# Optimization experiments

Hardware: AMD Instinct MI355X
Metric: run time of the kernel (lower is better)

Reference implementation:

```python
import jax, jax.numpy as jnp
import numpy as np

PADDING = 2  # matches init_kwargs; kernel_size = 2*PADDING + 1 -> no circular wrap in roll trick


def setup_inputs() -> dict:
    key = jax.random.key(0)
    k1, k2, k3 = jax.random.split(key, 3)
    x = jax.random.normal(k1, (16, 512, 4096), dtype=jnp.float32)
    weight = jax.random.normal(k2, (512, 512, 5), dtype=jnp.float32)
    bias = jax.random.normal(k3, (512,), dtype=jnp.float32)
    return {"x": x, "weight": weight, "bias": bias}


def reference(x, weight, bias):
    # Original torch module: pad(p,p) -> cat of roll(n-p) copies -> slice -> matmul.
    # Index algebra: out[b,o,t] = sum_{c,n} w[o,c,n] * xpad[b,c, t + 2p - n],
    # which (with kernel_size == 2p+1, so no circular wraparound) is a true
    # convolution, i.e. cross-correlation with the kernel flipped along taps.
    w_flipped = jnp.flip(weight, axis=-1)  # [O, I, K]
    y = jax.lax.conv_general_dilated(
        x, w_flipped,
        window_strides=(1,),
        padding=[(PADDING, PADDING)],
        dimension_numbers=("NCH", "OIH", "NCH"),
    )  # [B, O, T]
    return y + bias[None, :, None]
```

## Files before the change

kernel.cpp:

```cpp
#include <hip/hip_runtime.h>
#include <hip/hip_bf16.h>

typedef __attribute__((ext_vector_type(8))) short short8;
typedef __attribute__((ext_vector_type(4))) float f32x4;

#define B_   16
#define O_   512
#define C_   512
#define T_   4096
#define TP   (T_ + 32)
#define KT   5
#define BM   128
#define BN   512
#define BK   32
#define NCHUNK (C_/BK)
#define AFR  40
#define BGR  33

__device__ __forceinline__ void gload_lds16(const void* g, void* l) {
    __builtin_amdgcn_global_load_lds(
        (const __attribute__((address_space(1))) unsigned int*)g,
        (__attribute__((address_space(3))) unsigned int*)l, 16, 0, 0);
}

__global__ void prep_kernel(const float* __restrict__ w,
                            unsigned short* __restrict__ wb,
                            unsigned short* __restrict__ xt) {
    int bid = blockIdx.x;
    if (bid < 5120) {
        int e   = bid * 256 + threadIdx.x;
        int n   = e / (O_ * C_);
        int rem = e % (O_ * C_);
        int o   = rem / C_;
        int c   = rem % C_;
        float v = w[((size_t)o * C_ + c) * KT + n];
        __hip_bfloat16 h = __float2bfloat16(v);
        wb[e] = *reinterpret_cast<unsigned short*>(&h);
    } else {
        int i = (bid - 5120) * 256 + threadIdx.x;
        int b = i / (32 * C_);
        int r = (i / C_) % 32;
        int c = i % C_;
        int tp = (r < 16) ? r : (T_ + r);
        xt[((size_t)b * TP + tp) * C_ + c] = 0;
    }
}

__global__ void xtrans_kernel(const float* __restrict__ x, unsigned short* __restrict__ xt) {
    __shared__ float tile[64][65];
    int b  = blockIdx.z;
    int c0 = blockIdx.y * 64;
    int t0 = blockIdx.x * 64;
    const float* xb = x + ((size_t)b * C_ + c0) * T_ + t0;
#pragma unroll
    for (int p = 0; p < 4; ++p) {
        int idx = p * 256 + threadIdx.x;
        int cl = idx >> 4;
        int tj = (idx & 15) << 2;
        float4 v = *reinterpret_cast<const float4*>(xb + (size_t)cl * T_ + tj);
        tile[cl][tj + 0] = v.x;
        tile[cl][tj + 1] = v.y;
        tile[cl][tj + 2] = v.z;
        tile[cl][tj + 3] = v.w;
    }
    __syncthreads();
    unsigned short* xtb = xt + ((size_t)b * TP + 16 + t0) * C_ + c0;
#pragma unroll
    for (int p = 0; p < 2; ++p) {
        int g  = p * 256 + threadIdx.x;
        int tl = g >> 3;
        int cj = (g & 7) << 3;
        unsigned short tmp[8];
#pragma unroll
        for (int i = 0; i < 8; ++i) {
            __hip_bfloat16 h = __float2bfloat16(tile[cj + i][tl]);
            tmp[i] = *reinterpret_cast<unsigned short*>(&h);
        }
        *reinterpret_cast<short8*>(xtb + (size_t)tl * C_ + cj) =
            *reinterpret_cast<const short8*>(tmp);
    }
}

__global__ __launch_bounds__(512, 2) void conv_gemm_kernel(
        const unsigned short* __restrict__ wb,
        const unsigned short* __restrict__ xt,
        const float* __restrict__ bias,
        float* __restrict__ out) {
    __shared__ unsigned short a_lds[2][AFR * 512];
    __shared__ unsigned short b_lds[2][BGR * 512];

    int bid = blockIdx.x;
    int swz = (bid & 7) * 64 + (bid >> 3);
    int o0  = (swz & 3) * BM;
    int t0  = ((swz >> 2) & 7) * BN;
    int b   = swz >> 5;

    int tid  = threadIdx.x;
    int lane = tid & 63;
    int wid  = tid >> 6;
    int lr   = lane & 15;
    int lg   = lane >> 4;

    int bo[KT][4];
#pragma unroll
    for (int n = 0; n < KT; ++n)
#pragma unroll
        for (int ni = 0; ni < 4; ++ni) {
            int row = wid * 64 + ni * 16 + lr + 4 - n;
            bo[n][ni] = row * 32 + ((lg ^ ((row >> 1) & 3)) << 3);
        }

    f32x4 acc[8][4];
#pragma unroll
    for (int mi = 0; mi < 8; ++mi)
#pragma unroll
        for (int ni = 0; ni < 4; ++ni)
            acc[mi][ni] = (f32x4)0.0f;

    const unsigned short* ag = wb + (size_t)(o0 + lr) * C_ + lg * 8;
    int c8 = (lane & 3) ^ ((lane >> 3) & 3);
    const unsigned short* bg = xt + ((size_t)b * TP + (t0 + 14 + (lane >> 2))) * C_ + c8 * 8;

#pragma unroll
    for (int f = wid; f < AFR; f += 8)
        gload_lds16(ag + (size_t)((f >> 3) * O_ + (f & 7) * 16) * C_, &a_lds[0][f * 512]);
#pragma unroll
    for (int j = wid; j < BGR; j += 8)
        gload_lds16(bg + (size_t)(j * 16) * C_, &b_lds[0][j * 512]);
    asm volatile("s_waitcnt vmcnt(0)" ::: "memory");
    __builtin_amdgcn_s_barrier();

    for (int chunk = 0; chunk < NCHUNK; ++chunk) {
        int cur = chunk & 1;
        int c1  = (chunk + 1) * BK;
        bool pf = (chunk + 1 < NCHUNK);

#pragma unroll
        for (int n = 0; n < KT; ++n) {
            short8 af[8], bf[4];
#pragma unroll
            for (int mi = 0; mi < 8; ++mi)
                af[mi] = *reinterpret_cast<const short8*>(
                    &a_lds[cur][(n * 8 + mi) * 512 + lane * 8]);
#pragma unroll
            for (int ni = 0; ni < 4; ++ni)
                bf[ni] = *reinterpret_cast<const short8*>(&b_lds[cur][bo[n][ni]]);

            if (pf) {
                int f = n * 8 + wid;
                gload_lds16(ag + (size_t)((f >> 3) * O_ + (f & 7) * 16) * C_ + c1,
                            &a_lds[cur ^ 1][f * 512]);
                int j = n * 8 + wid;
                if (j < BGR)
                    gload_lds16(bg + (size_t)(j * 16) * C_ + c1, &b_lds[cur ^ 1][j * 512]);
            }

            __builtin_amdgcn_s_barrier();

            __builtin_amdgcn_s_setprio(1);
#pragma unroll
            for (int mi = 0; mi < 8; ++mi)
#pragma unroll
                for (int ni = 0; ni < 4; ++ni)
                    acc[mi][ni] = __builtin_amdgcn_mfma_f32_16x16x32_bf16(
                        af[mi], bf[ni], acc[mi][ni], 0, 0, 0);
            __builtin_amdgcn_s_setprio(0);
        }

        asm volatile("s_waitcnt vmcnt(0)" ::: "memory");
        __builtin_amdgcn_s_barrier();
    }

#pragma unroll
    for (int mi = 0; mi < 8; ++mi) {
#pragma unroll
        for (int ni = 0; ni < 4; ++ni) {
            int orow = o0 + mi * 16 + lg * 4;
            int tcol = t0 + wid * 64 + ni * 16 + lr;
#pragma unroll
            for (int r = 0; r < 4; ++r) {
                out[((size_t)b * O_ + orow + r) * T_ + tcol] =
                    acc[mi][ni][r] + bias[orow + r];
            }
        }
    }
}

extern "C" void kernel_launch(void* const* d_in, const int* in_sizes, int n_in,
                              void* d_out, int out_size, void* d_ws, size_t ws_size,
                              hipStream_t stream) {
    const float* x    = (const float*)d_in[0];
    const float* w    = (const float*)d_in[1];
    const float* bias = (const float*)d_in[2];
    float* out        = (float*)d_out;

    unsigned short* wb  = (unsigned short*)d_ws;
    unsigned short* xtp = wb + (size_t)KT * O_ * C_;

    prep_kernel<<<6144, 256, 0, stream>>>(w, wb, xtp);
    xtrans_kernel<<<dim3(T_ / 64, C_ / 64, B_), 256, 0, stream>>>(x, xtp);
    conv_gemm_kernel<<<512, 512, 0, stream>>>(wb, xtp, bias, out);
}
```

Baseline: 189.0 us.

## Retile conv GEMM to 256x256 blocks with 4-stage per-tap LDS pipeline

```diff
diff --git a/kernel.cpp b/kernel.cpp
--- a/kernel.cpp
+++ b/kernel.cpp
@@ -10,12 +10,7 @@
 #define T_   4096
 #define TP   (T_ + 32)
 #define KT   5
-#define BM   128
-#define BN   512
-#define BK   32
-#define NCHUNK (C_/BK)
-#define AFR  40
-#define BGR  33
+#define OC   (O_ * C_)
 
 __device__ __forceinline__ void gload_lds16(const void* g, void* l) {
     __builtin_amdgcn_global_load_lds(
@@ -29,8 +24,8 @@
     int bid = blockIdx.x;
     if (bid < 5120) {
         int e   = bid * 256 + threadIdx.x;
-        int n   = e / (O_ * C_);
-        int rem = e % (O_ * C_);
+        int n   = e / OC;
+        int rem = e % OC;
         int o   = rem / C_;
         int c   = rem % C_;
         float v = w[((size_t)o * C_ + c) * KT + n];
@@ -81,34 +76,95 @@
     }
 }
 
+#define VM8 asm volatile("s_waitcnt vmcnt(8)" ::: "memory")
+#define VM4 asm volatile("s_waitcnt vmcnt(4)" ::: "memory")
+#define VM0 asm volatile("s_waitcnt vmcnt(0)" ::: "memory")
+#define VMNONE
+
+#define HALF_BODY(SLOT, HN, DO_ISSUE, VMW)                                          \
+    {                                                                               \
+        const unsigned short* alp = &a_lds[SLOT][0];                                \
+        const unsigned short* blp = &b_lds[SLOT][0];                                \
+        short8 af[8], bf[4];                                                        \
+        _Pragma("unroll")                                                           \
+        for (int mi = 0; mi < 4; ++mi)                                              \
+            af[mi] = *reinterpret_cast<const short8*>(&alp[ao[mi]]);                \
+        _Pragma("unroll")                                                           \
+        for (int ni = 0; ni < 4; ++ni)                                              \
+            bf[ni] = *reinterpret_cast<const short8*>(&blp[bo[ni]]);                \
+        if (DO_ISSUE) {                                                             \
+            int H3  = (HN) + 3;                                                     \
+            int j3  = H3 >> 1;                                                      \
+            int n3  = j3 >> 3;                                                      \
+            size_t off3 = (size_t)(((j3 & 7) << 6) + ((H3 & 1) << 5));              \
+            unsigned short* ad = &a_lds[((SLOT) + 3) & 3][wid * 1024];              \
+            unsigned short* bd = &b_lds[((SLOT) + 3) & 3][wid * 1024];              \
+            const unsigned short* as = agl + (size_t)n3 * OC + off3;                \
+            const unsigned short* bs = bgl + (ptrdiff_t)(2 - n3) * C_ + off3;       \
+            gload_lds16(as, ad);                                                    \
+            gload_lds16(as + 16 * C_, ad + 512);                                    \
+            gload_lds16(bs, bd);                                                    \
+            gload_lds16(bs + 16 * C_, bd + 512);                                    \
+        }                                                                           \
+        __builtin_amdgcn_s_barrier();                                               \
+        __builtin_amdgcn_s_setprio(1);                                              \
+        _Pragma("unroll")                                                           \
+        for (int mi = 0; mi < 4; ++mi)                                              \
+            _Pragma("unroll")                                                       \
+            for (int ni = 0; ni < 4; ++ni)                                          \
+                acc[mi][ni] = __builtin_amdgcn_mfma_f32_16x16x32_bf16(              \
+                    af[mi], bf[ni], acc[mi][ni], 0, 0, 0);                          \
+        __builtin_amdgcn_s_setprio(0);                                              \
+        __builtin_amdgcn_s_barrier();                                               \
+        _Pragma("unroll")                                                           \
+        for (int mi = 4; mi < 8; ++mi)                                              \
+            af[mi] = *reinterpret_cast<const short8*>(&alp[ao[mi]]);                \
+        __builtin_amdgcn_s_barrier();                                               \
+        __builtin_amdgcn_s_setprio(1);                                              \
+        _Pragma("unroll")                                                           \
+        for (int mi = 4; mi < 8; ++mi)                                              \
+            _Pragma("unroll")                                                       \
+            for (int ni = 0; ni < 4; ++ni)                                          \
+                acc[mi][ni] = __builtin_amdgcn_mfma_f32_16x16x32_bf16(              \
+                    af[mi], bf[ni], acc[mi][ni], 0, 0, 0);                          \
+        __builtin_amdgcn_s_setprio(0);                                              \
+        VMW;                                                                        \
+        __builtin_amdgcn_s_barrier();                                               \
+    }
+
 __global__ __launch_bounds__(512, 2) void conv_gemm_kernel(
         const unsigned short* __restrict__ wb,
         const unsigned short* __restrict__ xt,
         const float* __restrict__ bias,
         float* __restrict__ out) {
-    __shared__ unsigned short a_lds[2][AFR * 512];
-    __shared__ unsigned short b_lds[2][BGR * 512];
+    __shared__ unsigned short a_lds[4][8192];
+    __shared__ unsigned short b_lds[4][8192];
 
     int bid = blockIdx.x;
     int swz = (bid & 7) * 64 + (bid >> 3);
-    int o0  = (swz & 3) * BM;
-    int t0  = ((swz >> 2) & 7) * BN;
+    int o0  = (swz & 1) * 256;
+    int t0  = ((swz >> 1) & 15) * 256;
     int b   = swz >> 5;
 
     int tid  = threadIdx.x;
     int lane = tid & 63;
     int wid  = tid >> 6;
+    int wm   = wid >> 2;
+    int wn   = wid & 3;
     int lr   = lane & 15;
     int lg   = lane >> 4;
 
-    int bo[KT][4];
-#pragma unroll
-    for (int n = 0; n < KT; ++n)
-#pragma unroll
-        for (int ni = 0; ni < 4; ++ni) {
-            int row = wid * 64 + ni * 16 + lr + 4 - n;
-            bo[n][ni] = row * 32 + ((lg ^ ((row >> 1) & 3)) << 3);
-        }
+    int ao[8], bo[4];
+#pragma unroll
+    for (int mi = 0; mi < 8; ++mi) {
+        int row = wm * 128 + mi * 16 + lr;
+        ao[mi] = row * 32 + ((lg ^ ((row >> 1) & 3)) << 3);
+    }
+#pragma unroll
+    for (int ni = 0; ni < 4; ++ni) {
+        int row = wn * 64 + ni * 16 + lr;
+        bo[ni] = row * 32 + ((lg ^ ((row >> 1) & 3)) << 3);
+    }
 
     f32x4 acc[8][4];
 #pragma unroll
@@ -117,66 +173,46 @@
         for (int ni = 0; ni < 4; ++ni)
             acc[mi][ni] = (f32x4)0.0f;
 
-    const unsigned short* ag = wb + (size_t)(o0 + lr) * C_ + lg * 8;
     int c8 = (lane & 3) ^ ((lane >> 3) & 3);
-    const unsigned short* bg = xt + ((size_t)b * TP + (t0 + 14 + (lane >> 2))) * C_ + c8 * 8;
-
-#pragma unroll
-    for (int f = wid; f < AFR; f += 8)
-        gload_lds16(ag + (size_t)((f >> 3) * O_ + (f & 7) * 16) * C_, &a_lds[0][f * 512]);
-#pragma unroll
-    for (int j = wid; j < BGR; j += 8)
-        gload_lds16(bg + (size_t)(j * 16) * C_, &b_lds[0][j * 512]);
-    asm volatile("s_waitcnt vmcnt(0)" ::: "memory");
+    const unsigned short* agl =
+        wb + (size_t)(o0 + wid * 32 + (lane >> 2)) * C_ + c8 * 8;
+    const unsigned short* bgl =
+        xt + ((size_t)b * TP + 16 + t0 + wid * 32 + (lane >> 2)) * C_ + c8 * 8;
+
+#pragma unroll
+    for (int h = 0; h < 3; ++h) {
+        size_t off = (size_t)(((h >> 1) << 6) + ((h & 1) << 5));
+        unsigned short* ad = &a_lds[h][wid * 1024];
+        unsigned short* bd = &b_lds[h][wid * 1024];
+        const unsigned short* as = agl + off;
+        const unsigned short* bs = bgl + 2 * C_ + off;
+        gload_lds16(as, ad);
+        gload_lds16(as + 16 * C_, ad + 512);
+        gload_lds16(bs, bd);
+        gload_lds16(bs + 16 * C_, bd + 512);
+    }
+    VM8;
     __builtin_amdgcn_s_barrier();
 
-    for (int chunk = 0; chunk < NCHUNK; ++chunk) {
-        int cur = chunk & 1;
-        int c1  = (chunk + 1) * BK;
-        bool pf = (chunk + 1 < NCHUNK);
-
-#pragma unroll
-        for (int n = 0; n < KT; ++n) {
-            short8 af[8], bf[4];
-#pragma unroll
-            for (int mi = 0; mi < 8; ++mi)
-                af[mi] = *reinterpret_cast<const short8*>(
-                    &a_lds[cur][(n * 8 + mi) * 512 + lane * 8]);
-#pragma unroll
-            for (int ni = 0; ni < 4; ++ni)
-                bf[ni] = *reinterpret_cast<const short8*>(&b_lds[cur][bo[n][ni]]);
-
-            if (pf) {
-                int f = n * 8 + wid;
-                gload_lds16(ag + (size_t)((f >> 3) * O_ + (f & 7) * 16) * C_ + c1,
-                            &a_lds[cur ^ 1][f * 512]);
-                int j = n * 8 + wid;
-                if (j < BGR)
-                    gload_lds16(bg + (size_t)(j * 16) * C_ + c1, &b_lds[cur ^ 1][j * 512]);
-            }
-
-            __builtin_amdgcn_s_barrier();
-
-            __builtin_amdgcn_s_setprio(1);
-#pragma unroll
-            for (int mi = 0; mi < 8; ++mi)
-#pragma unroll
-                for (int ni = 0; ni < 4; ++ni)
-                    acc[mi][ni] = __builtin_amdgcn_mfma_f32_16x16x32_bf16(
-                        af[mi], bf[ni], acc[mi][ni], 0, 0, 0);
-            __builtin_amdgcn_s_setprio(0);
-        }
-
-        asm volatile("s_waitcnt vmcnt(0)" ::: "memory");
-        __builtin_amdgcn_s_barrier();
-    }
+#pragma unroll 1
+    for (int hg = 0; hg < 19; ++hg) {
+        int H = hg * 4;
+        HALF_BODY(0, H + 0, 1, VM8);
+        HALF_BODY(1, H + 1, 1, VM8);
+        HALF_BODY(2, H + 2, 1, VM8);
+        HALF_BODY(3, H + 3, 1, VM8);
+    }
+    HALF_BODY(0, 76, 1, VM8);
+    HALF_BODY(1, 77, 0, VM4);
+    HALF_BODY(2, 78, 0, VM0);
+    HALF_BODY(3, 79, 0, VMNONE);
 
 #pragma unroll
     for (int mi = 0; mi < 8; ++mi) {
 #pragma unroll
         for (int ni = 0; ni < 4; ++ni) {
-            int orow = o0 + mi * 16 + lg * 4;
-            int tcol = t0 + wid * 64 + ni * 16 + lr;
+            int orow = o0 + wm * 128 + mi * 16 + lg * 4;
+            int tcol = t0 + wn * 64 + ni * 16 + lr;
 #pragma unroll
             for (int r = 0; r < 4; ++r) {
                 out[((size_t)b * O_ + orow + r) * T_ + tcol] =
@@ -195,7 +231,7 @@
     float* out        = (float*)d_out;
 
     unsigned short* wb  = (unsigned short*)d_ws;
-    unsigned short* xtp = wb + (size_t)KT * O_ * C_;
+    unsigned short* xtp = wb + (size_t)KT * OC;
 
     prep_kernel<<<6144, 256, 0, stream>>>(w, wb, xtp);
     xtrans_kernel<<<dim3(T_ / 64, C_ / 64, B_), 256, 0, stream>>>(x, xtp);
```

Result: slower. 219.8 us (+16.3%).

## Replace full vmcnt drain with per-tap counted waits in conv GEMM pipeline

Applied to the files above, without the earlier changes.

```diff
diff --git a/kernel.cpp b/kernel.cpp
--- a/kernel.cpp
+++ b/kernel.cpp
@@ -22,6 +22,9 @@
         (const __attribute__((address_space(1))) unsigned int*)g,
         (__attribute__((address_space(3))) unsigned int*)l, 16, 0, 0);
 }
+
+#define VMW_(N) asm volatile("s_waitcnt vmcnt(" #N ")" ::: "memory")
+#define VMW(N)  VMW_(N)
 
 __global__ void prep_kernel(const float* __restrict__ w,
                             unsigned short* __restrict__ wb,
@@ -81,6 +84,40 @@
     }
 }
 
+#define PHASE(n, VMN, PF)                                                           \
+    {                                                                               \
+        if (PF) {                                                                   \
+            if ((n) == 0) {                                                         \
+                _Pragma("unroll")                                                   \
+                for (int k = 0; k < 4; ++k)                                         \
+                    gload_lds16(bg + (size_t)((wid + 8 * k) * 16) * C_ + c1,        \
+                                &b_lds[nxt][(wid + 8 * k) * 512]);                  \
+                gload_lds16(bg + (size_t)(je * 16) * C_ + c1,                       \
+                            &b_lds[nxt][je * 512]);                                 \
+            }                                                                       \
+            gload_lds16(ag + (size_t)((n) * O_ + wid * 16) * C_ + c1,               \
+                        &a_lds[nxt][((n) * 8 + wid) * 512]);                        \
+        }                                                                           \
+        VMW(VMN);                                                                   \
+        __builtin_amdgcn_s_barrier();                                               \
+        short8 af[8], bf[4];                                                        \
+        _Pragma("unroll")                                                           \
+        for (int mi = 0; mi < 8; ++mi)                                              \
+            af[mi] = *reinterpret_cast<const short8*>(                              \
+                &a_lds[cur][((n) * 8 + mi) * 512 + lane * 8]);                      \
+        _Pragma("unroll")                                                           \
+        for (int ni = 0; ni < 4; ++ni)                                              \
+            bf[ni] = *reinterpret_cast<const short8*>(&b_lds[cur][bo[(n)][ni]]);    \
+        __builtin_amdgcn_s_setprio(1);                                              \
+        _Pragma("unroll")                                                           \
+        for (int mi = 0; mi < 8; ++mi)                                              \
+            _Pragma("unroll")                                                       \
+            for (int ni = 0; ni < 4; ++ni)                                          \
+                acc[mi][ni] = __builtin_amdgcn_mfma_f32_16x16x32_bf16(              \
+                    af[mi], bf[ni], acc[mi][ni], 0, 0, 0);                          \
+        __builtin_amdgcn_s_setprio(0);                                              \
+    }
+
 __global__ __launch_bounds__(512, 2) void conv_gemm_kernel(
         const unsigned short* __restrict__ wb,
         const unsigned short* __restrict__ xt,
@@ -100,6 +137,7 @@
     int wid  = tid >> 6;
     int lr   = lane & 15;
     int lg   = lane >> 4;
+    int je   = (wid == 0) ? 32 : (23 + wid);
 
     int bo[KT][4];
 #pragma unroll
@@ -122,53 +160,34 @@
     const unsigned short* bg = xt + ((size_t)b * TP + (t0 + 14 + (lane >> 2))) * C_ + c8 * 8;
 
 #pragma unroll
-    for (int f = wid; f < AFR; f += 8)
-        gload_lds16(ag + (size_t)((f >> 3) * O_ + (f & 7) * 16) * C_, &a_lds[0][f * 512]);
-#pragma unroll
-    for (int j = wid; j < BGR; j += 8)
-        gload_lds16(bg + (size_t)(j * 16) * C_, &b_lds[0][j * 512]);
-    asm volatile("s_waitcnt vmcnt(0)" ::: "memory");
-    __builtin_amdgcn_s_barrier();
-
-    for (int chunk = 0; chunk < NCHUNK; ++chunk) {
+    for (int k = 0; k < 4; ++k)
+        gload_lds16(bg + (size_t)((wid + 8 * k) * 16) * C_, &b_lds[0][(wid + 8 * k) * 512]);
+    gload_lds16(bg + (size_t)(je * 16) * C_, &b_lds[0][je * 512]);
+#pragma unroll
+    for (int n = 0; n < KT; ++n)
+        gload_lds16(ag + (size_t)(n * O_ + wid * 16) * C_, &a_lds[0][(n * 8 + wid) * 512]);
+
+    for (int chunk = 0; chunk < NCHUNK - 1; ++chunk) {
         int cur = chunk & 1;
+        int nxt = cur ^ 1;
         int c1  = (chunk + 1) * BK;
-        bool pf = (chunk + 1 < NCHUNK);
-
-#pragma unroll
-        for (int n = 0; n < KT; ++n) {
-            short8 af[8], bf[4];
-#pragma unroll
-            for (int mi = 0; mi < 8; ++mi)
-                af[mi] = *reinterpret_cast<const short8*>(
-                    &a_lds[cur][(n * 8 + mi) * 512 + lane * 8]);
-#pragma unroll
-            for (int ni = 0; ni < 4; ++ni)
-                bf[ni] = *reinterpret_cast<const short8*>(&b_lds[cur][bo[n][ni]]);
-
-            if (pf) {
-                int f = n * 8 + wid;
-                gload_lds16(ag + (size_t)((f >> 3) * O_ + (f & 7) * 16) * C_ + c1,
-                            &a_lds[cur ^ 1][f * 512]);
-                int j = n * 8 + wid;
-                if (j < BGR)
-                    gload_lds16(bg + (size_t)(j * 16) * C_ + c1, &b_lds[cur ^ 1][j * 512]);
-            }
-
-            __builtin_amdgcn_s_barrier();
-
-            __builtin_amdgcn_s_setprio(1);
-#pragma unroll
-            for (int mi = 0; mi < 8; ++mi)
-#pragma unroll
-                for (int ni = 0; ni < 4; ++ni)
-                    acc[mi][ni] = __builtin_amdgcn_mfma_f32_16x16x32_bf16(
-                        af[mi], bf[ni], acc[mi][ni], 0, 0, 0);
-            __builtin_amdgcn_s_setprio(0);
-        }
-
-        asm volatile("s_waitcnt vmcnt(0)" ::: "memory");
+        PHASE(0, 10, 1)
+        PHASE(1, 10, 1)
+        PHASE(2, 10, 1)
+        PHASE(3, 10, 1)
+        PHASE(4, 10, 1)
         __builtin_amdgcn_s_barrier();
+    }
+    {
+        int cur = (NCHUNK - 1) & 1;
+        int nxt = cur ^ 1;
+        int c1  = 0;
+        (void)nxt; (void)c1;
+        PHASE(0, 4, 0)
+        PHASE(1, 3, 0)
+        PHASE(2, 2, 0)
+        PHASE(3, 1, 0)
+        PHASE(4, 0, 0)
     }
 
 #pragma unroll
```

Measured after the change: 190.4 us. Within noise of the previous version (+0.7%).

## Double-buffer A fragments in registers and software-pipeline LDS reads with MFMAs

Applied to the files above, without the earlier changes.

```diff
diff --git a/kernel.cpp b/kernel.cpp
--- a/kernel.cpp
+++ b/kernel.cpp
@@ -81,6 +81,71 @@
     }
 }
 
+#define BARR __builtin_amdgcn_s_barrier()
+#define SB0  __builtin_amdgcn_sched_barrier(0)
+
+#define LDB(TAP, BUF)                                                       \
+    _Pragma("unroll")                                                       \
+    for (int ni = 0; ni < 4; ++ni) {                                        \
+        int row = rb + (ni * 16 - (TAP));                                   \
+        int off = row * 32 + ((lg ^ ((row >> 1) & 3)) << 3);                \
+        bf[ni] = *reinterpret_cast<const short8*>(&b_lds[BUF][off]);        \
+    }
+
+#define LDA(SET, TAP, BUF)                                                  \
+    _Pragma("unroll")                                                       \
+    for (int mi = 0; mi < 8; ++mi)                                          \
+        af[SET][mi] = *reinterpret_cast<const short8*>(                     \
+            &a_lds[BUF][((TAP) * 8 + mi) * 512 + lane * 8]);
+
+#define MFMAS(SET)                                                          \
+    __builtin_amdgcn_s_setprio(1);                                          \
+    _Pragma("unroll")                                                       \
+    for (int mi = 0; mi < 8; ++mi)                                          \
+        _Pragma("unroll")                                                   \
+        for (int ni = 0; ni < 4; ++ni)                                      \
+            acc[mi][ni] = __builtin_amdgcn_mfma_f32_16x16x32_bf16(          \
+                af[SET][mi], bf[ni], acc[mi][ni], 0, 0, 0);                 \
+    __builtin_amdgcn_s_setprio(0);
+
+#define GLA(K, DB) gload_lds16(ag + (size_t)((K) * O_ + wid * 16) * C_ + c1,   \
+                               &a_lds[DB][((K) * 8 + wid) * 512])
+#define GLB(J, DB) gload_lds16(bg + (size_t)((J) * 16) * C_ + c1,              \
+                               &b_lds[DB][(J) * 512])
+
+#define CHUNK_BODY(CH, PAR)                                                    \
+    {                                                                          \
+        int c1  = ((CH) + 1) * BK;                                             \
+        bool pf = ((CH) + 1 < NCHUNK);                                         \
+                                                                      \
+        LDB(0, PAR); LDA((1 + PAR) & 1, 1, PAR);                               \
+        if (pf) { GLA(0, (PAR) ^ 1); GLA(1, (PAR) ^ 1); GLB(wid, (PAR) ^ 1); } \
+        BARR; SB0; MFMAS((0 + PAR) & 1);                                       \
+                                                                      \
+        LDB(1, PAR); LDA((2 + PAR) & 1, 2, PAR);                               \
+        if (pf) { GLA(2, (PAR) ^ 1); GLA(3, (PAR) ^ 1); GLB(8 + wid, (PAR) ^ 1); } \
+        BARR; SB0; MFMAS((1 + PAR) & 1);                                       \
+                                                                      \
+        LDB(2, PAR); LDA((3 + PAR) & 1, 3, PAR);                               \
+        if (pf) { GLA(4, (PAR) ^ 1); GLB(16 + wid, (PAR) ^ 1); GLB(24 + wid, (PAR) ^ 1); } \
+        BARR; SB0; MFMAS((2 + PAR) & 1);                                       \
+                                                                      \
+        LDB(3, PAR); LDA((4 + PAR) & 1, 4, PAR);                               \
+        if (pf && wid == 0) GLB(32, (PAR) ^ 1);                                \
+        BARR; SB0; MFMAS((3 + PAR) & 1);                                       \
+                                                      \
+        if (pf) {                                                              \
+            asm volatile("s_waitcnt vmcnt(0)" ::: "memory");                   \
+            BARR; SB0;                                                         \
+            LDB(4, PAR); LDA((5 + PAR) & 1, 0, (PAR) ^ 1);                     \
+            asm volatile("s_waitcnt lgkmcnt(8)" ::: "memory"); SB0;            \
+            BARR; SB0;                                                         \
+        } else {                                                               \
+            LDB(4, PAR);                                                       \
+        }                                                                      \
+        MFMAS((4 + PAR) & 1);                                                  \
+    }
+
 __global__ __launch_bounds__(512, 2) void conv_gemm_kernel(
         const unsigned short* __restrict__ wb,
         const unsigned short* __restrict__ xt,
@@ -100,15 +165,7 @@
     int wid  = tid >> 6;
     int lr   = lane & 15;
     int lg   = lane >> 4;
-
-    int bo[KT][4];
-#pragma unroll
-    for (int n = 0; n < KT; ++n)
-#pragma unroll
-        for (int ni = 0; ni < 4; ++ni) {
-            int row = wid * 64 + ni * 16 + lr + 4 - n;
-            bo[n][ni] = row * 32 + ((lg ^ ((row >> 1) & 3)) << 3);
-        }
+    int rb   = wid * 64 + lr + 4;
 
     f32x4 acc[8][4];
 #pragma unroll
@@ -121,54 +178,28 @@
     int c8 = (lane & 3) ^ ((lane >> 3) & 3);
     const unsigned short* bg = xt + ((size_t)b * TP + (t0 + 14 + (lane >> 2))) * C_ + c8 * 8;
 
-#pragma unroll
-    for (int f = wid; f < AFR; f += 8)
-        gload_lds16(ag + (size_t)((f >> 3) * O_ + (f & 7) * 16) * C_, &a_lds[0][f * 512]);
-#pragma unroll
-    for (int j = wid; j < BGR; j += 8)
-        gload_lds16(bg + (size_t)(j * 16) * C_, &b_lds[0][j * 512]);
+    short8 af[2][8];
+    short8 bf[4];
+
+    {
+        int c1 = 0;
+#pragma unroll
+        for (int f = wid; f < AFR; f += 8)
+            gload_lds16(ag + (size_t)((f >> 3) * O_ + (f & 7) * 16) * C_, &a_lds[0][f * 512]);
+#pragma unroll
+        for (int j = wid; j < BGR; j += 8)
+            gload_lds16(bg + (size_t)(j * 16) * C_, &b_lds[0][j * 512]);
+        (void)c1;
+    }
     asm volatile("s_waitcnt vmcnt(0)" ::: "memory");
-    __builtin_amdgcn_s_barrier();
-
-    for (int chunk = 0; chunk < NCHUNK; ++chunk) {
-        int cur = chunk & 1;
-        int c1  = (chunk + 1) * BK;
-        bool pf = (chunk + 1 < NCHUNK);
-
-#pragma unroll
-        for (int n = 0; n < KT; ++n) {
-            short8 af[8], bf[4];
-#pragma unroll
-            for (int mi = 0; mi < 8; ++mi)
-                af[mi] = *reinterpret_cast<const short8*>(
-                    &a_lds[cur][(n * 8 + mi) * 512 + lane * 8]);
-#pragma unroll
-            for (int ni = 0; ni < 4; ++ni)
-                bf[ni] = *reinterpret_cast<const short8*>(&b_lds[cur][bo[n][ni]]);
-
-            if (pf) {
-                int f = n * 8 + wid;
-                gload_lds16(ag + (size_t)((f >> 3) * O_ + (f & 7) * 16) * C_ + c1,
-                            &a_lds[cur ^ 1][f * 512]);
-                int j = n * 8 + wid;
-                if (j < BGR)
-                    gload_lds16(bg + (size_t)(j * 16) * C_ + c1, &b_lds[cur ^ 1][j * 512]);
-            }
-
-            __builtin_amdgcn_s_barrier();
-
-            __builtin_amdgcn_s_setprio(1);
-#pragma unroll
-            for (int mi = 0; mi < 8; ++mi)
-#pragma unroll
-                for (int ni = 0; ni < 4; ++ni)
-                    acc[mi][ni] = __builtin_amdgcn_mfma_f32_16x16x32_bf16(
-                        af[mi], bf[ni], acc[mi][ni], 0, 0, 0);
-            __builtin_amdgcn_s_setprio(0);
-        }
-
-        asm volatile("s_waitcnt vmcnt(0)" ::: "memory");
-        __builtin_amdgcn_s_barrier();
+    BARR;
+    LDA(0, 0, 0);
+
+#pragma unroll 1
+    for (int cp = 0; cp < NCHUNK / 2; ++cp) {
+        int ch = cp * 2;
+        CHUNK_BODY(ch, 0);
+        CHUNK_BODY(ch + 1, 1);
     }
 
 #pragma unroll
```

New measurement: 247.2 us. 30.8% more time.
